# Kernel tuning notes

Hardware: AMD Instinct MI355X
Metric: run time of the kernel (lower is better)

Reference implementation:

```python
import jax, jax.numpy as jnp
import numpy as np

B, H, E, K, O = 16384, 4096, 8, 2, 1
H2 = H // 2


def setup_inputs() -> dict:
    key = jax.random.key(0)
    ks = jax.random.split(key, 9)
    s_h = 1.0 / np.sqrt(H)
    s_h2 = 1.0 / np.sqrt(H2)
    return {
        "x": jax.random.normal(ks[0], (B, H), dtype=jnp.float32),
        # stacked expert weights
        "We1": jax.random.uniform(ks[1], (E, H, H2), jnp.float32, -s_h, s_h),
        "be1": jax.random.uniform(ks[2], (E, H2), jnp.float32, -s_h, s_h),
        "We2": jax.random.uniform(ks[3], (E, H2, O), jnp.float32, -s_h2, s_h2),
        "be2": jax.random.uniform(ks[4], (E, O), jnp.float32, -s_h2, s_h2),
        # gate weights
        "Wg1": jax.random.uniform(ks[5], (H, H2), jnp.float32, -s_h, s_h),
        "bg1": jax.random.uniform(ks[6], (H2,), jnp.float32, -s_h, s_h),
        "Wg2": jax.random.uniform(ks[7], (H2, E), jnp.float32, -s_h2, s_h2),
        "bg2": jax.random.uniform(ks[8], (E,), jnp.float32, -s_h2, s_h2),
    }


def reference(x, We1, be1, We2, be2, Wg1, bg1, Wg2, bg2):
    # gating: Linear -> ReLU -> Linear -> softmax (dropout is identity in eval)
    gh = jax.nn.relu(x @ Wg1 + bg1)                      # [B, H2]
    gate_probs = jax.nn.softmax(gh @ Wg2 + bg2, axis=-1)  # [B, E]
    top_p, top_idx = jax.lax.top_k(gate_probs, K)        # [B, K]
    top_p = top_p / jnp.sum(top_p, axis=-1, keepdims=True)
    # dense all-experts MLP (faithful to original's redundant compute)
    h = jax.nn.relu(jnp.einsum('bh,ehd->bed', x, We1) + be1)  # [B, E, H2]
    expert_out = jnp.einsum('bed,edo->beo', h, We2) + be2     # [B, E, O]
    # gather top-k experts per token and combine
    sel = jnp.take_along_axis(expert_out, top_idx[:, :, None], axis=1)  # [B, K, O]
    return jnp.sum(sel * top_p[:, :, None], axis=1)  # [B, O]
```

## Files before the change

### kernel.cpp

```cpp
#include <hip/hip_runtime.h>
#include <hip/hip_bf16.h>
#include <stdint.h>


#define B_DIM  16384
#define H_DIM  4096
#define H2_DIM 2048
#define E_DIM  8

typedef __attribute__((ext_vector_type(8))) short short8;
typedef __attribute__((ext_vector_type(4))) float f32x4;

static __device__ __forceinline__ unsigned int bf16_rn(float f) {
    unsigned int u = __builtin_bit_cast(unsigned int, f);
    u += 0x7FFFu + ((u >> 16) & 1u);
    return u >> 16;
}
static __device__ __forceinline__ float bf16f(unsigned int h) {
    unsigned int u = h << 16;
    return __builtin_bit_cast(float, u);
}

static __device__ __forceinline__ void gload_lds16(const void* g, void* l) {
    __builtin_amdgcn_global_load_lds(
        (const __attribute__((address_space(1))) unsigned int*)g,
        (__attribute__((address_space(3))) unsigned int*)l,
        16, 0, 0);
}

__global__ __launch_bounds__(256) void build_xA_panels(
    const float* __restrict__ x, unsigned short* __restrict__ panA)
{
    const int t = blockIdx.x, bm = blockIdx.y, tid = threadIdx.x;
    const size_t ubase = (size_t)(bm * 64 + t) * 2 * 8192;
#pragma unroll
    for (int u = 0; u < 8; ++u) {
        const int gid = u * 256 + tid;
        const int h = gid >> 10, rem = gid & 1023;
        const int row = rem >> 2, slot = rem & 3;
        const int kslot = slot ^ ((row >> 1) & 3);
        const float* s = x + (size_t)(bm * 256 + row) * H_DIM
                           + t * 64 + h * 32 + kslot * 8;
        f32x4 a = ((const f32x4*)s)[0], b = ((const f32x4*)s)[1];
        uint4 o;
        o.x = bf16_rn(a[0]) | (bf16_rn(a[1]) << 16);
        o.y = bf16_rn(a[2]) | (bf16_rn(a[3]) << 16);
        o.z = bf16_rn(b[0]) | (bf16_rn(b[1]) << 16);
        o.w = bf16_rn(b[2]) | (bf16_rn(b[3]) << 16);
        *(uint4*)(panA + ubase + (size_t)h * 8192 + row * 32 + slot * 8) = o;
    }
}

__global__ __launch_bounds__(256) void build_xA_panels_hl(
    const float* __restrict__ x, unsigned short* __restrict__ panA,
    unsigned short* __restrict__ panAl)
{
    const int t = blockIdx.x, bm = blockIdx.y, tid = threadIdx.x;
    const size_t ubase = (size_t)(bm * 64 + t) * 2 * 8192;
#pragma unroll
    for (int u = 0; u < 8; ++u) {
        const int gid = u * 256 + tid;
        const int h = gid >> 10, rem = gid & 1023;
        const int row = rem >> 2, slot = rem & 3;
        const int kslot = slot ^ ((row >> 1) & 3);
        const float* s = x + (size_t)(bm * 256 + row) * H_DIM
                           + t * 64 + h * 32 + kslot * 8;
        f32x4 a = ((const f32x4*)s)[0], b = ((const f32x4*)s)[1];
        unsigned int hb[8], lb[8];
        float v[8] = {a[0], a[1], a[2], a[3], b[0], b[1], b[2], b[3]};
#pragma unroll
        for (int q = 0; q < 8; ++q) {
            hb[q] = bf16_rn(v[q]);
            lb[q] = bf16_rn(v[q] - bf16f(hb[q]));
        }
        uint4 oh, ol;
        oh.x = hb[0] | (hb[1] << 16); oh.y = hb[2] | (hb[3] << 16);
        oh.z = hb[4] | (hb[5] << 16); oh.w = hb[6] | (hb[7] << 16);
        ol.x = lb[0] | (lb[1] << 16); ol.y = lb[2] | (lb[3] << 16);
        ol.z = lb[4] | (lb[5] << 16); ol.w = lb[6] | (lb[7] << 16);
        const size_t idx = ubase + (size_t)h * 8192 + row * 32 + slot * 8;
        *(uint4*)(panA + idx)  = oh;
        *(uint4*)(panAl + idx) = ol;
    }
}

__global__ __launch_bounds__(256) void build_w1B_panels(
    const float* __restrict__ We1, unsigned short* __restrict__ panB)
{
    __shared__ unsigned short tile[64][72];
    const int dblk = blockIdx.x, t = blockIdx.y, e = blockIdx.z;
    const int tid = threadIdx.x;
    {
        const int kr = tid >> 2, c0 = (tid & 3) * 16;
        const float* s = We1 + ((size_t)e * H_DIM + t * 64 + kr) * H2_DIM
                             + dblk * 64 + c0;
#pragma unroll
        for (int q = 0; q < 4; ++q) {
            f32x4 v = ((const f32x4*)s)[q];
            tile[kr][c0 + q * 4 + 0] = (unsigned short)bf16_rn(v[0]);
            tile[kr][c0 + q * 4 + 1] = (unsigned short)bf16_rn(v[1]);
            tile[kr][c0 + q * 4 + 2] = (unsigned short)bf16_rn(v[2]);
            tile[kr][c0 + q * 4 + 3] = (unsigned short)bf16_rn(v[3]);
        }
    }
    __syncthreads();
    const int nbG = e * 8 + (dblk >> 2);
    const int col = tid >> 2, slot = tid & 3;
    const int colg = (dblk & 3) * 64 + col;
    const int kslot = slot ^ ((colg >> 1) & 3);
#pragma unroll
    for (int hh = 0; hh < 2; ++hh) {
        const int kl = hh * 32 + kslot * 8;
        uint4 o;
        o.x = (unsigned int)tile[kl + 0][col] | ((unsigned int)tile[kl + 1][col] << 16);
        o.y = (unsigned int)tile[kl + 2][col] | ((unsigned int)tile[kl + 3][col] << 16);
        o.z = (unsigned int)tile[kl + 4][col] | ((unsigned int)tile[kl + 5][col] << 16);
        o.w = (unsigned int)tile[kl + 6][col] | ((unsigned int)tile[kl + 7][col] << 16);
        *(uint4*)(panB + (((size_t)nbG * 64 + t) * 2 + hh) * 8192
                        + colg * 32 + slot * 8) = o;
    }
}

__global__ __launch_bounds__(256) void build_wg1_panels(
    const float* __restrict__ Wg1, unsigned short* __restrict__ panBgh,
    unsigned short* __restrict__ panBgl)
{
    __shared__ unsigned short tileH[64][72];
    __shared__ unsigned short tileL[64][72];
    const int dblk = blockIdx.x, t = blockIdx.y;
    const int tid = threadIdx.x;
    {
        const int kr = tid >> 2, c0 = (tid & 3) * 16;
        const float* s = Wg1 + ((size_t)t * 64 + kr) * H2_DIM + dblk * 64 + c0;
#pragma unroll
        for (int q = 0; q < 4; ++q) {
            f32x4 v = ((const f32x4*)s)[q];
#pragma unroll
            for (int j = 0; j < 4; ++j) {
                const unsigned int hb = bf16_rn(v[j]);
                tileH[kr][c0 + q * 4 + j] = (unsigned short)hb;
                tileL[kr][c0 + q * 4 + j] =
                    (unsigned short)bf16_rn(v[j] - bf16f(hb));
            }
        }
    }
    __syncthreads();
    const int nbG = dblk >> 1;
    const int col = tid >> 2, slot = tid & 3;
    const int colg = (dblk & 1) * 64 + col;
    const int kslot = slot ^ ((colg >> 1) & 3);
#pragma unroll
    for (int hh = 0; hh < 2; ++hh) {
        const int kl = hh * 32 + kslot * 8;
        uint4 oh, ol;
        oh.x = (unsigned int)tileH[kl + 0][col] | ((unsigned int)tileH[kl + 1][col] << 16);
        oh.y = (unsigned int)tileH[kl + 2][col] | ((unsigned int)tileH[kl + 3][col] << 16);
        oh.z = (unsigned int)tileH[kl + 4][col] | ((unsigned int)tileH[kl + 5][col] << 16);
        oh.w = (unsigned int)tileH[kl + 6][col] | ((unsigned int)tileH[kl + 7][col] << 16);
        ol.x = (unsigned int)tileL[kl + 0][col] | ((unsigned int)tileL[kl + 1][col] << 16);
        ol.y = (unsigned int)tileL[kl + 2][col] | ((unsigned int)tileL[kl + 3][col] << 16);
        ol.z = (unsigned int)tileL[kl + 4][col] | ((unsigned int)tileL[kl + 5][col] << 16);
        ol.w = (unsigned int)tileL[kl + 6][col] | ((unsigned int)tileL[kl + 7][col] << 16);
        const size_t idx = (((size_t)nbG * 64 + t) * 2 + hh) * 4096
                         + colg * 32 + slot * 8;
        *(uint4*)(panBgh + idx) = oh;
        *(uint4*)(panBgl + idx) = ol;
    }
}

__global__ __launch_bounds__(256, 3) void moe_gate_panel(
    const unsigned short* __restrict__ panA, const unsigned short* __restrict__ panAl,
    const unsigned short* __restrict__ panBgh, const unsigned short* __restrict__ panBgl,
    const float* __restrict__ bg1, const float* __restrict__ Wg2,
    float* __restrict__ gpart)
{
    __shared__ short lAh[4096], lAl[4096];
    __shared__ short lBh[4096], lBl[4096];
    __shared__ float lW2[128 * 8];
    __shared__ float gred[2][128][8];

    const int tid  = threadIdx.x;
    const int lane = tid & 63;
    const int wv   = tid >> 6;
    const int wm   = wv >> 1;
    const int wn   = wv & 1;
    const int nb = blockIdx.x;
    const int bm = blockIdx.y;
    const int dbase = nb * 128;

    const char* AhB = (const char*)panA  + ((size_t)(bm >> 1) << 21)
                                         + ((size_t)(bm & 1) << 13);
    const char* AlB = (const char*)panAl + ((size_t)(bm >> 1) << 21)
                                         + ((size_t)(bm & 1) << 13);
    const char* BhB = (const char*)panBgh + ((size_t)nb << 20);
    const char* BlB = (const char*)panBgl + ((size_t)nb << 20);

    {
        const f32x4* s = reinterpret_cast<const f32x4*>(Wg2 + (size_t)dbase * 8);
        reinterpret_cast<f32x4*>(lW2)[tid] = s[tid];
    }

    const int rA = wm * 64 + (lane & 15);
    const int offA = rA * 64 + ((((lane >> 4)) ^ ((rA >> 1) & 3)) << 4);
    const int rB = wn * 64 + (lane & 15);
    const int offB = rB * 64 + ((((lane >> 4)) ^ ((rB >> 1) & 3)) << 4);

    f32x4 acc[4][4];
#pragma unroll
    for (int i = 0; i < 4; ++i)
#pragma unroll
        for (int j = 0; j < 4; ++j) acc[i][j] = (f32x4){0.f, 0.f, 0.f, 0.f};

#define GRD8(BASE, OFF) \
    (*reinterpret_cast<const short8*>(reinterpret_cast<const char*>(BASE) + (OFF)))

    for (int t = 0; t < 128; ++t) {
        __syncthreads();
        {
            const char* ua = AhB + ((size_t)t << 14);
            gload_lds16(ua + tid * 16,        (char*)lAh + wv * 1024);
            gload_lds16(ua + 4096 + tid * 16, (char*)lAh + 4096 + wv * 1024);
            const char* ul = AlB + ((size_t)t << 14);
            gload_lds16(ul + tid * 16,        (char*)lAl + wv * 1024);
            gload_lds16(ul + 4096 + tid * 16, (char*)lAl + 4096 + wv * 1024);
            const char* ub = BhB + ((size_t)t << 13);
            gload_lds16(ub + tid * 16,        (char*)lBh + wv * 1024);
            gload_lds16(ub + 4096 + tid * 16, (char*)lBh + 4096 + wv * 1024);
            const char* vb = BlB + ((size_t)t << 13);
            gload_lds16(vb + tid * 16,        (char*)lBl + wv * 1024);
            gload_lds16(vb + 4096 + tid * 16, (char*)lBl + 4096 + wv * 1024);
        }
        __syncthreads();

        short8 ah[4], al[4], bh[4], bl[4];
#pragma unroll
        for (int i = 0; i < 4; ++i) {
            ah[i] = GRD8(lAh, offA + i * 1024);
            al[i] = GRD8(lAl, offA + i * 1024);
        }
#pragma unroll
        for (int n = 0; n < 4; ++n) {
            bh[n] = GRD8(lBh, offB + n * 1024);
            bl[n] = GRD8(lBl, offB + n * 1024);
        }
        __builtin_amdgcn_s_setprio(1);
#pragma unroll
        for (int i = 0; i < 4; ++i)
#pragma unroll
            for (int n = 0; n < 4; ++n) {
                acc[i][n] = __builtin_amdgcn_mfma_f32_16x16x32_bf16(ah[i], bh[n], acc[i][n], 0, 0, 0);
                acc[i][n] = __builtin_amdgcn_mfma_f32_16x16x32_bf16(ah[i], bl[n], acc[i][n], 0, 0, 0);
                acc[i][n] = __builtin_amdgcn_mfma_f32_16x16x32_bf16(al[i], bh[n], acc[i][n], 0, 0, 0);
            }
        __builtin_amdgcn_s_setprio(0);
    }
#undef GRD8

    const int c = lane & 15, g = lane >> 4;
    float bgv[4];
#pragma unroll
    for (int ni = 0; ni < 4; ++ni) bgv[ni] = bg1[dbase + wn * 64 + ni * 16 + c];
#pragma unroll
    for (int mi = 0; mi < 4; ++mi) {
#pragma unroll
        for (int r = 0; r < 4; ++r) {
            float gv[4];
#pragma unroll
            for (int ni = 0; ni < 4; ++ni)
                gv[ni] = fmaxf(acc[mi][ni][r] + bgv[ni], 0.f);
#pragma unroll
            for (int e8 = 0; e8 < 8; ++e8) {
                float tsum = 0.f;
#pragma unroll
                for (int ni = 0; ni < 4; ++ni)
                    tsum = fmaf(gv[ni], lW2[(wn * 64 + ni * 16 + c) * 8 + e8], tsum);
                tsum += __shfl_xor(tsum, 1);
                tsum += __shfl_xor(tsum, 2);
                tsum += __shfl_xor(tsum, 4);
                tsum += __shfl_xor(tsum, 8);
                if (c == e8) gred[wn][wm * 64 + mi * 16 + g * 4 + r][e8] = tsum;
            }
        }
    }
    __syncthreads();
    {
        const int row = tid & 127;
        const int ebase = (tid >> 7) * 4;
        const int b = bm * 128 + row;
#pragma unroll
        for (int i = 0; i < 4; ++i) {
            const int e8 = ebase + i;
            gpart[(size_t)b * 128 + nb * 8 + e8] =
                gred[0][row][e8] + gred[1][row][e8];
        }
    }
}

__global__ void route_zero(int* __restrict__ cnt) {
    if (threadIdx.x < E_DIM) cnt[threadIdx.x] = 0;
}

__global__ __launch_bounds__(256) void moe_logits_topk(
    const float* __restrict__ gpart, const float* __restrict__ bg2,
    int* __restrict__ sel, float* __restrict__ w2f,
    int* __restrict__ cnt, int* __restrict__ tokenlist)
{
    const int b = blockIdx.x * 256 + threadIdx.x;
    float logit[8];
#pragma unroll
    for (int e = 0; e < 8; ++e) logit[e] = bg2[e];
    const float* gp = gpart + (size_t)b * 128;
#pragma unroll
    for (int cN = 0; cN < 16; ++cN)
#pragma unroll
        for (int e = 0; e < 8; ++e) logit[e] += gp[cN * 8 + e];

    int i1 = 0; float m1 = logit[0];
#pragma unroll
    for (int e = 1; e < 8; ++e) if (logit[e] > m1) { m1 = logit[e]; i1 = e; }
    int i2 = -1; float m2 = -3.4e38f;
#pragma unroll
    for (int e = 0; e < 8; ++e) if (e != i1 && logit[e] > m2) { m2 = logit[e]; i2 = e; }

    sel[b] = i1 | (i2 << 8);
    w2f[b] = expf(m2 - m1);
    const int p1 = atomicAdd(&cnt[i1], 1);
    tokenlist[i1 * B_DIM + p1] = (b << 1);
    const int p2 = atomicAdd(&cnt[i2], 1);
    tokenlist[i2 * B_DIM + p2] = (b << 1) | 1;
}

__global__ void moe_tiletab(
    const int* __restrict__ cnt, int* __restrict__ tileE,
    int* __restrict__ tileB, int* __restrict__ nTiles)
{
    if (threadIdx.x == 0) {
        int tot = 0;
        for (int e = 0; e < E_DIM; ++e) {
            const int nt = (cnt[e] + 127) >> 7;
            for (int j = 0; j < nt; ++j) { tileE[tot] = e; tileB[tot] = j; ++tot; }
        }
        *nTiles = tot;
    }
}

__global__ __launch_bounds__(512, 4) void moe_expert_sparse(
    const unsigned short* __restrict__ panA, const unsigned short* __restrict__ panB,
    const float* __restrict__ be1, const float* __restrict__ We2,
    const int* __restrict__ tileE, const int* __restrict__ tileB,
    const int* __restrict__ nTiles, const int* __restrict__ cnt,
    const int* __restrict__ tokenlist, float* __restrict__ esel)
{
    __shared__ short lA[3][4096];
    __shared__ short lB[3][8192];
    __shared__ float red[4][128];
    __shared__ int   tokbuf[128];

    const int tix = blockIdx.y;
    if (tix >= *nTiles) return;
    const int chunk = blockIdx.x;

    const int tid  = threadIdx.x;
    const int lane = tid & 63;
    const int wv   = tid >> 6;
    const int wm   = wv >> 2;
    const int wn   = wv & 3;

    const int e  = tileE[tix];
    const int tb = tileB[tix];
    const int ce = cnt[e];
    const int nb = e * 8 + chunk;
    const int dbase = chunk * 256;

    if (tid < 128) {
        const int gi = tb * 128 + tid;
        tokbuf[tid] = (gi < ce) ? tokenlist[e * B_DIM + gi] : -1;
    }
    __syncthreads();

    const int rawT = tokbuf[tid >> 2];
    const int tokv = ((rawT < 0) ? tokbuf[0] : rawT) >> 1;
    const int trow = tokv & 255;
    const int lr = tid >> 2, ls = tid & 3;
    const int sslot = ls ^ ((lr >> 1) & 3) ^ ((trow >> 1) & 3);
    const char* Asrc = (const char*)panA + ((size_t)(tokv >> 8) << 21)
                     + trow * 64 + sslot * 16;
    const char* Bbase = (const char*)panB + ((size_t)nb << 21);

#define STAGE(TT, CC) do {                                                     \
    gload_lds16(Asrc + ((size_t)(TT) << 14), (char*)&lA[CC][0] + wv * 1024);   \
    const char* ub_ = Bbase + ((size_t)(TT) << 14);                            \
    gload_lds16(ub_ + tid * 16, (char*)&lB[CC][0] + wv * 1024);                \
    gload_lds16(ub_ + 8192 + tid * 16, (char*)&lB[CC][0] + 8192 + wv * 1024);  \
} while (0)

#define RD8(BASE, OFF) \
    (*reinterpret_cast<const short8*>(reinterpret_cast<const char*>(BASE) + (OFF)))

    const int rA = wm * 64 + (lane & 15);
    const int offA = rA * 64 + ((((lane >> 4)) ^ ((rA >> 1) & 3)) << 4);
    const int rB = wn * 64 + (lane & 15);
    const int offB = rB * 64 + ((((lane >> 4)) ^ ((rB >> 1) & 3)) << 4);

    f32x4 acc[4][4];
#pragma unroll
    for (int i = 0; i < 4; ++i)
#pragma unroll
        for (int j = 0; j < 4; ++j) acc[i][j] = (f32x4){0.f, 0.f, 0.f, 0.f};

    STAGE(0, 0);
    STAGE(1, 1);
    asm volatile("s_waitcnt vmcnt(3)");
    __builtin_amdgcn_s_barrier();

#define ITER(CUR, NXT, TN) do {                                                \
    STAGE(TN, NXT);                                                            \
    short8 af_[4], bf_[4];                                                     \
    _Pragma("unroll")                                                          \
    for (int i = 0; i < 4; ++i) af_[i] = RD8(&lA[CUR][0], offA + i * 1024);    \
    _Pragma("unroll")                                                          \
    for (int n = 0; n < 4; ++n) bf_[n] = RD8(&lB[CUR][0], offB + n * 1024);    \
    __builtin_amdgcn_s_setprio(1);                                             \
    _Pragma("unroll")                                                          \
    for (int i = 0; i < 4; ++i)                                                \
        _Pragma("unroll")                                                      \
        for (int n = 0; n < 4; ++n)                                            \
            acc[i][n] = __builtin_amdgcn_mfma_f32_16x16x32_bf16(af_[i], bf_[n], acc[i][n], 0, 0, 0); \
    __builtin_amdgcn_s_setprio(0);                                             \
    asm volatile("s_waitcnt vmcnt(3)");                                        \
    __builtin_amdgcn_s_barrier();                                              \
} while (0)

    for (int t = 0; t < 126; t += 3) {
        ITER(0, 2, t + 2);
        ITER(1, 0, t + 3);
        ITER(2, 1, t + 4);
    }
    ITER(0, 2, 127);
    ITER(1, 0, 127);
    asm volatile("s_waitcnt vmcnt(0)");
#undef ITER
#undef STAGE

    const int cc = lane & 15, g = lane >> 4;
    float w2v[4], b1v[4];
#pragma unroll
    for (int ni = 0; ni < 4; ++ni) {
        const int d = dbase + wn * 64 + ni * 16 + cc;
        b1v[ni] = be1[e * H2_DIM + d];
        w2v[ni] = We2[e * H2_DIM + d];
    }
#pragma unroll
    for (int mi = 0; mi < 4; ++mi) {
#pragma unroll
        for (int r = 0; r < 4; ++r) {
            float s = 0.f;
#pragma unroll
            for (int ni = 0; ni < 4; ++ni) {
                float v = acc[mi][ni][r] + b1v[ni];
                v = fmaxf(v, 0.f);
                s = fmaf(v, w2v[ni], s);
            }
            s += __shfl_xor(s, 1);
            s += __shfl_xor(s, 2);
            s += __shfl_xor(s, 4);
            s += __shfl_xor(s, 8);
            if (cc == 0) red[wn][wm * 64 + mi * 16 + g * 4 + r] = s;
        }
    }
    __syncthreads();
    if (tid < 128) {
        const int r2 = tokbuf[tid];
        if (r2 >= 0) {
            const int tk = r2 >> 1, sl = r2 & 1;
            esel[(size_t)tk * 16 + sl * 8 + chunk] =
                red[0][tid] + red[1][tid] + red[2][tid] + red[3][tid];
        }
    }
}

__global__ __launch_bounds__(256) void moe_finalize_sparse(
    const float* __restrict__ esel, const int* __restrict__ sel,
    const float* __restrict__ w2f, const float* __restrict__ be2,
    float* __restrict__ out)
{
    const int b = blockIdx.x * 256 + threadIdx.x;
    const int s = sel[b];
    const int i1 = s & 255, i2 = (s >> 8) & 255;
    const float w2 = w2f[b];
    const float* ep = esel + (size_t)b * 16;
    float eo1 = be2[i1], eo2 = be2[i2];
#pragma unroll
    for (int c = 0; c < 8; ++c) eo1 += ep[c];
#pragma unroll
    for (int c = 0; c < 8; ++c) eo2 += ep[8 + c];
    out[b] = (eo1 + w2 * eo2) / (1.f + w2);
}

__global__ __launch_bounds__(512, 4) void moe_expert_gemm_128(
    const unsigned short* __restrict__ panA, const unsigned short* __restrict__ panB,
    const float* __restrict__ be1, const float* __restrict__ We2,
    float* __restrict__ epart)
{
    __shared__ short lA[3][4096];
    __shared__ short lB[3][8192];
    __shared__ float red[4][128];

    const int tid  = threadIdx.x;
    const int lane = tid & 63;
    const int wv   = tid >> 6;
    const int wm   = wv >> 2;
    const int wn   = wv & 3;

    const int lin = blockIdx.x;
    const int sb  = lin >> 8, i5 = lin & 255;
    const int sbm = sb & 7, snb = sb >> 3;
    const int xcd = i5 & 7, j5 = i5 >> 3;
    const int bm  = sbm * 16 + (xcd & 1) * 8 + (j5 & 7);
    const int nb  = snb * 16 + (xcd >> 1) * 4 + (j5 >> 3);
    const int e = nb >> 3, chunk = nb & 7;
    const int dbase = chunk * 256;

    const char* Abase = (const char*)panA + ((size_t)(bm >> 1) << 21)
                                          + ((size_t)(bm & 1) << 13);
    const char* Bbase = (const char*)panB + ((size_t)nb << 21);

#define STAGE(TT, CC) do {                                                     \
    const char* ua_ = Abase + ((size_t)(TT) << 14);                            \
    gload_lds16(ua_ + tid * 16, (char*)&lA[CC][0] + wv * 1024);                \
    const char* ub_ = Bbase + ((size_t)(TT) << 14);                            \
    gload_lds16(ub_ + tid * 16, (char*)&lB[CC][0] + wv * 1024);                \
    gload_lds16(ub_ + 8192 + tid * 16, (char*)&lB[CC][0] + 8192 + wv * 1024);  \
} while (0)

#define RD8(BASE, OFF) \
    (*reinterpret_cast<const short8*>(reinterpret_cast<const char*>(BASE) + (OFF)))

    const int rA = wm * 64 + (lane & 15);
    const int offA = rA * 64 + ((((lane >> 4)) ^ ((rA >> 1) & 3)) << 4);
    const int rB = wn * 64 + (lane & 15);
    const int offB = rB * 64 + ((((lane >> 4)) ^ ((rB >> 1) & 3)) << 4);

    f32x4 acc[4][4];
#pragma unroll
    for (int i = 0; i < 4; ++i)
#pragma unroll
        for (int j = 0; j < 4; ++j) acc[i][j] = (f32x4){0.f, 0.f, 0.f, 0.f};

    STAGE(0, 0);
    STAGE(1, 1);
    asm volatile("s_waitcnt vmcnt(3)");
    __builtin_amdgcn_s_barrier();

#define ITER(CUR, NXT, TN) do {                                                \
    STAGE(TN, NXT);                                                            \
    short8 af_[4], bf_[4];                                                     \
    _Pragma("unroll")                                                          \
    for (int i = 0; i < 4; ++i) af_[i] = RD8(&lA[CUR][0], offA + i * 1024);    \
    _Pragma("unroll")                                                          \
    for (int n = 0; n < 4; ++n) bf_[n] = RD8(&lB[CUR][0], offB + n * 1024);    \
    __builtin_amdgcn_s_setprio(1);                                             \
    _Pragma("unroll")                                                          \
    for (int i = 0; i < 4; ++i)                                                \
        _Pragma("unroll")                                                      \
        for (int n = 0; n < 4; ++n)                                            \
            acc[i][n] = __builtin_amdgcn_mfma_f32_16x16x32_bf16(af_[i], bf_[n], acc[i][n], 0, 0, 0); \
    __builtin_amdgcn_s_setprio(0);                                             \
    asm volatile("s_waitcnt vmcnt(3)");                                        \
    __builtin_amdgcn_s_barrier();                                              \
} while (0)

    for (int t = 0; t < 126; t += 3) {
        ITER(0, 2, t + 2);
        ITER(1, 0, t + 3);
        ITER(2, 1, t + 4);
    }
    ITER(0, 2, 127);
    ITER(1, 0, 127);
    asm volatile("s_waitcnt vmcnt(0)");
#undef ITER
#undef STAGE

    const int cc = lane & 15, g = lane >> 4;
    float w2v[4], b1v[4];
#pragma unroll
    for (int ni = 0; ni < 4; ++ni) {
        const int d = dbase + wn * 64 + ni * 16 + cc;
        b1v[ni] = be1[e * H2_DIM + d];
        w2v[ni] = We2[e * H2_DIM + d];
    }
#pragma unroll
    for (int mi = 0; mi < 4; ++mi) {
#pragma unroll
        for (int r = 0; r < 4; ++r) {
            float s = 0.f;
#pragma unroll
            for (int ni = 0; ni < 4; ++ni) {
                float v = acc[mi][ni][r] + b1v[ni];
                v = fmaxf(v, 0.f);
                s = fmaf(v, w2v[ni], s);
            }
            s += __shfl_xor(s, 1);
            s += __shfl_xor(s, 2);
            s += __shfl_xor(s, 4);
            s += __shfl_xor(s, 8);
            if (cc == 0) red[wn][wm * 64 + mi * 16 + g * 4 + r] = s;
        }
    }
    __syncthreads();
    if (tid < 128) {
        const int b = bm * 128 + tid;
        epart[((size_t)b * E_DIM + e) * 8 + chunk] =
            red[0][tid] + red[1][tid] + red[2][tid] + red[3][tid];
    }
}

__global__ __launch_bounds__(256, 2) void moe_gate_gemm(
    const float* __restrict__ x, const float* __restrict__ Wg1,
    const float* __restrict__ bg1, const float* __restrict__ Wg2,
    float* __restrict__ gpart)
{
    __shared__ short lAh[128 * 64], lAl[128 * 64];
    __shared__ short lBh[128 * 64], lBl[128 * 64];
    __shared__ float lW2[128 * 8];
    __shared__ float gred[2][128][8];

    const int tid  = threadIdx.x;
    const int lane = tid & 63;
    const int wm = (tid >> 6) >> 1, wn = (tid >> 6) & 1;
    const int nb = blockIdx.x, bm = blockIdx.y;
    const int dbase = nb * 128;

    const float* Asrc = x + (size_t)bm * 128 * H_DIM;
    const float* Bsrc = Wg1 + dbase;

    {
        const f32x4* s = reinterpret_cast<const f32x4*>(Wg2 + (size_t)dbase * 8);
        reinterpret_cast<f32x4*>(lW2)[tid] = s[tid];
    }

    f32x4 acc[4][4];
#pragma unroll
    for (int i = 0; i < 4; ++i)
#pragma unroll
        for (int j = 0; j < 4; ++j) acc[i][j] = (f32x4){0.f, 0.f, 0.f, 0.f};

    const int arow0 = tid >> 4, af4 = tid & 15;
    const int bn = tid & 127, bkc0 = tid >> 7;

    for (int k0 = 0; k0 < H_DIM; k0 += 64) {
        __syncthreads();
#pragma unroll
        for (int j = 0; j < 8; ++j) {
            const int row = arow0 + j * 16;
            const float* p = Asrc + (size_t)row * H_DIM + k0 + af4 * 4;
            float a[4] = {p[0], p[1], p[2], p[3]};
            unsigned int hb[4], lb[4];
#pragma unroll
            for (int q = 0; q < 4; ++q) {
                hb[q] = bf16_rn(a[q]);
                lb[q] = bf16_rn(a[q] - bf16f(hb[q]));
            }
            const int byte = row * 128 + ((af4 * 8) ^ ((row & 7) << 4));
            *reinterpret_cast<uint2*>(reinterpret_cast<char*>(lAh) + byte) =
                make_uint2(hb[0] | (hb[1] << 16), hb[2] | (hb[3] << 16));
            *reinterpret_cast<uint2*>(reinterpret_cast<char*>(lAl) + byte) =
                make_uint2(lb[0] | (lb[1] << 16), lb[2] | (lb[3] << 16));
        }
#pragma unroll
        for (int j = 0; j < 4; ++j) {
            const int kc = bkc0 + 2 * j;
            const float* p = Bsrc + (size_t)(k0 + kc * 8) * H2_DIM + bn;
            unsigned int hb[8], lb[8];
#pragma unroll
            for (int q = 0; q < 8; ++q) {
                float v = p[(size_t)q * H2_DIM];
                hb[q] = bf16_rn(v);
                lb[q] = bf16_rn(v - bf16f(hb[q]));
            }
            const int byte = bn * 128 + ((kc * 16) ^ ((bn & 7) << 4));
            *reinterpret_cast<uint4*>(reinterpret_cast<char*>(lBh) + byte) =
                make_uint4(hb[0] | (hb[1] << 16), hb[2] | (hb[3] << 16),
                           hb[4] | (hb[5] << 16), hb[6] | (hb[7] << 16));
            *reinterpret_cast<uint4*>(reinterpret_cast<char*>(lBl) + byte) =
                make_uint4(lb[0] | (lb[1] << 16), lb[2] | (lb[3] << 16),
                           lb[4] | (lb[5] << 16), lb[6] | (lb[7] << 16));
        }
        __syncthreads();
#pragma unroll
        for (int kk = 0; kk < 2; ++kk) {
            const int kbyte = kk * 64 + ((lane >> 4) << 4);
            short8 ah[4], al[4], bh[4], bl[4];
#pragma unroll
            for (int mi = 0; mi < 4; ++mi) {
                const int r = wm * 64 + mi * 16 + (lane & 15);
                const int off = r * 128 + (kbyte ^ ((r & 7) << 4));
                ah[mi] = *reinterpret_cast<const short8*>(reinterpret_cast<const char*>(lAh) + off);
                al[mi] = *reinterpret_cast<const short8*>(reinterpret_cast<const char*>(lAl) + off);
            }
#pragma unroll
            for (int ni = 0; ni < 4; ++ni) {
                const int r = wn * 64 + ni * 16 + (lane & 15);
                const int off = r * 128 + (kbyte ^ ((r & 7) << 4));
                bh[ni] = *reinterpret_cast<const short8*>(reinterpret_cast<const char*>(lBh) + off);
                bl[ni] = *reinterpret_cast<const short8*>(reinterpret_cast<const char*>(lBl) + off);
            }
#pragma unroll
            for (int mi = 0; mi < 4; ++mi)
#pragma unroll
                for (int ni = 0; ni < 4; ++ni) {
                    acc[mi][ni] = __builtin_amdgcn_mfma_f32_16x16x32_bf16(ah[mi], bh[ni], acc[mi][ni], 0, 0, 0);
                    acc[mi][ni] = __builtin_amdgcn_mfma_f32_16x16x32_bf16(ah[mi], bl[ni], acc[mi][ni], 0, 0, 0);
                    acc[mi][ni] = __builtin_amdgcn_mfma_f32_16x16x32_bf16(al[mi], bh[ni], acc[mi][ni], 0, 0, 0);
                }
        }
    }

    const int c = lane & 15, g = lane >> 4;
    float bgv[4];
#pragma unroll
    for (int ni = 0; ni < 4; ++ni) bgv[ni] = bg1[dbase + wn * 64 + ni * 16 + c];
#pragma unroll
    for (int mi = 0; mi < 4; ++mi) {
#pragma unroll
        for (int r = 0; r < 4; ++r) {
            float gv[4];
#pragma unroll
            for (int ni = 0; ni < 4; ++ni)
                gv[ni] = fmaxf(acc[mi][ni][r] + bgv[ni], 0.f);
#pragma unroll
            for (int e8 = 0; e8 < 8; ++e8) {
                float t = 0.f;
#pragma unroll
                for (int ni = 0; ni < 4; ++ni)
                    t = fmaf(gv[ni], lW2[(wn * 64 + ni * 16 + c) * 8 + e8], t);
                t += __shfl_xor(t, 1);
                t += __shfl_xor(t, 2);
                t += __shfl_xor(t, 4);
                t += __shfl_xor(t, 8);
                if (c == e8) gred[wn][wm * 64 + mi * 16 + g * 4 + r][e8] = t;
            }
        }
    }
    __syncthreads();
    {
        const int row = tid & 127;
        const int ebase = (tid >> 7) * 4;
        const int b = bm * 128 + row;
#pragma unroll
        for (int i = 0; i < 4; ++i) {
            const int e8 = ebase + i;
            gpart[(size_t)b * 128 + nb * 8 + e8] = gred[0][row][e8] + gred[1][row][e8];
        }
    }
}

__global__ __launch_bounds__(256, 2) void moe_expert_gemm(
    const float* __restrict__ x, const float* __restrict__ We1,
    const float* __restrict__ be1, const float* __restrict__ We2,
    float* __restrict__ epart)
{
    __shared__ short lA[128 * 64];
    __shared__ short lB[128 * 64];
    __shared__ float red[2][128];

    const int tid  = threadIdx.x;
    const int lane = tid & 63;
    const int wm   = (tid >> 6) >> 1;
    const int wn   = (tid >> 6) & 1;
    const int nb = blockIdx.x, bm = blockIdx.y;
    const int e = nb >> 4, chunk = nb & 15;
    const int dbase = chunk * 128;

    const float* Asrc = x + (size_t)bm * 128 * H_DIM;
    const float* Bsrc = We1 + (size_t)e * H_DIM * H2_DIM + dbase;

    f32x4 acc[4][4];
#pragma unroll
    for (int i = 0; i < 4; ++i)
#pragma unroll
        for (int j = 0; j < 4; ++j) acc[i][j] = (f32x4){0.f, 0.f, 0.f, 0.f};

    const int arow0 = tid >> 4, af4 = tid & 15;
    const int bn = tid & 127, bkc0 = tid >> 7;

    for (int k0 = 0; k0 < H_DIM; k0 += 64) {
        __syncthreads();
#pragma unroll
        for (int j = 0; j < 8; ++j) {
            const int row = arow0 + j * 16;
            const float* p = Asrc + (size_t)row * H_DIM + k0 + af4 * 4;
            float a0 = p[0], a1 = p[1], a2 = p[2], a3 = p[3];
            uint2 wv2;
            wv2.x = bf16_rn(a0) | (bf16_rn(a1) << 16);
            wv2.y = bf16_rn(a2) | (bf16_rn(a3) << 16);
            const int byte = row * 128 + ((af4 * 8) ^ ((row & 7) << 4));
            *reinterpret_cast<uint2*>(reinterpret_cast<char*>(lA) + byte) = wv2;
        }
#pragma unroll
        for (int j = 0; j < 4; ++j) {
            const int kc = bkc0 + 2 * j;
            const float* p = Bsrc + (size_t)(k0 + kc * 8) * H2_DIM + bn;
            uint4 wv4;
            wv4.x = bf16_rn(p[0])          | (bf16_rn(p[H2_DIM])     << 16);
            wv4.y = bf16_rn(p[2 * H2_DIM]) | (bf16_rn(p[3 * H2_DIM]) << 16);
            wv4.z = bf16_rn(p[4 * H2_DIM]) | (bf16_rn(p[5 * H2_DIM]) << 16);
            wv4.w = bf16_rn(p[6 * H2_DIM]) | (bf16_rn(p[7 * H2_DIM]) << 16);
            const int byte = bn * 128 + ((kc * 16) ^ ((bn & 7) << 4));
            *reinterpret_cast<uint4*>(reinterpret_cast<char*>(lB) + byte) = wv4;
        }
        __syncthreads();
#pragma unroll
        for (int kk = 0; kk < 2; ++kk) {
            const int kbyte = kk * 64 + ((lane >> 4) << 4);
            short8 af[4], bfr[4];
#pragma unroll
            for (int mi = 0; mi < 4; ++mi) {
                const int r = wm * 64 + mi * 16 + (lane & 15);
                af[mi] = *reinterpret_cast<const short8*>(
                    reinterpret_cast<const char*>(lA) + r * 128 + (kbyte ^ ((r & 7) << 4)));
            }
#pragma unroll
            for (int ni = 0; ni < 4; ++ni) {
                const int r = wn * 64 + ni * 16 + (lane & 15);
                bfr[ni] = *reinterpret_cast<const short8*>(
                    reinterpret_cast<const char*>(lB) + r * 128 + (kbyte ^ ((r & 7) << 4)));
            }
#pragma unroll
            for (int mi = 0; mi < 4; ++mi)
#pragma unroll
                for (int ni = 0; ni < 4; ++ni)
                    acc[mi][ni] = __builtin_amdgcn_mfma_f32_16x16x32_bf16(
                        af[mi], bfr[ni], acc[mi][ni], 0, 0, 0);
        }
    }

    const int c = lane & 15, g = lane >> 4;
    float w2v[4], b1v[4];
#pragma unroll
    for (int ni = 0; ni < 4; ++ni) {
        const int d = dbase + wn * 64 + ni * 16 + c;
        b1v[ni] = be1[e * H2_DIM + d];
        w2v[ni] = We2[e * H2_DIM + d];
    }
#pragma unroll
    for (int mi = 0; mi < 4; ++mi) {
#pragma unroll
        for (int r = 0; r < 4; ++r) {
            float s = 0.f;
#pragma unroll
            for (int ni = 0; ni < 4; ++ni) {
                float v = acc[mi][ni][r] + b1v[ni];
                v = fmaxf(v, 0.f);
                s = fmaf(v, w2v[ni], s);
            }
            s += __shfl_xor(s, 1);
            s += __shfl_xor(s, 2);
            s += __shfl_xor(s, 4);
            s += __shfl_xor(s, 8);
            if (c == 0) red[wn][wm * 64 + mi * 16 + g * 4 + r] = s;
        }
    }
    __syncthreads();
    if (tid < 128) {
        const int b = bm * 128 + tid;
        epart[((size_t)b * E_DIM + e) * 16 + chunk] = red[0][tid] + red[1][tid];
    }
}

template <int NC>
__global__ __launch_bounds__(256) void moe_finalize(
    const float* __restrict__ gpart, const float* __restrict__ epart,
    const float* __restrict__ bg2, const float* __restrict__ be2,
    float* __restrict__ out)
{
    const int b = blockIdx.x * 256 + threadIdx.x;
    float logit[8];
#pragma unroll
    for (int e = 0; e < 8; ++e) logit[e] = bg2[e];
    const float* gp = gpart + (size_t)b * 128;
#pragma unroll
    for (int cN = 0; cN < 16; ++cN)
#pragma unroll
        for (int e = 0; e < 8; ++e) logit[e] += gp[cN * 8 + e];

    float eo[8];
    const float* ep = epart + (size_t)b * E_DIM * NC;
#pragma unroll
    for (int e = 0; e < 8; ++e) {
        float s = be2[e];
#pragma unroll
        for (int cN = 0; cN < NC; ++cN) s += ep[e * NC + cN];
        eo[e] = s;
    }

    int i1 = 0; float m1 = logit[0];
#pragma unroll
    for (int e = 1; e < 8; ++e) if (logit[e] > m1) { m1 = logit[e]; i1 = e; }
    int i2 = -1; float m2 = -3.4e38f;
#pragma unroll
    for (int e = 0; e < 8; ++e) if (e != i1 && logit[e] > m2) { m2 = logit[e]; i2 = e; }

    const float w2 = expf(m2 - m1);
    out[b] = (eo[i1] + w2 * eo[i2]) / (1.f + w2);
}

extern "C" void kernel_launch(void* const* d_in, const int* in_sizes, int n_in,
                              void* d_out, int out_size, void* d_ws, size_t ws_size,
                              hipStream_t stream) {
    (void)in_sizes; (void)n_in; (void)out_size;
    const float* x   = (const float*)d_in[0];
    const float* We1 = (const float*)d_in[1];
    const float* be1 = (const float*)d_in[2];
    const float* We2 = (const float*)d_in[3];
    const float* be2 = (const float*)d_in[4];
    const float* Wg1 = (const float*)d_in[5];
    const float* bg1 = (const float*)d_in[6];
    const float* Wg2 = (const float*)d_in[7];
    const float* bg2 = (const float*)d_in[8];
    float* out = (float*)d_out;

    char* ws = (char*)d_ws;
    size_t off = 0;
    float* gpart = (float*)(ws + off);                  off += (size_t)B_DIM * 128 * 4;
    float* epart = (float*)(ws + off);                  off += (size_t)B_DIM * 128 * 4;
    unsigned short* panA = (unsigned short*)(ws + off); off += (size_t)B_DIM * H_DIM * 2;
    unsigned short* panB = (unsigned short*)(ws + off); off += (size_t)E_DIM * H2_DIM * H_DIM * 2;
    const size_t NEED2 = off;
    unsigned short* panAl  = (unsigned short*)(ws + off); off += (size_t)B_DIM * H_DIM * 2;
    unsigned short* panBgh = (unsigned short*)(ws + off); off += (size_t)H2_DIM * H_DIM * 2;
    unsigned short* panBgl = (unsigned short*)(ws + off); off += (size_t)H2_DIM * H_DIM * 2;
    int*   cnt       = (int*)(ws + off);   off += 256;
    int*   nTiles    = (int*)(ws + off);   off += 256;
    int*   tileE     = (int*)(ws + off);   off += 272 * 4;
    int*   tileB     = (int*)(ws + off);   off += 272 * 4;
    int*   sel       = (int*)(ws + off);   off += (size_t)B_DIM * 4;
    float* w2f       = (float*)(ws + off); off += (size_t)B_DIM * 4;
    int*   tokenlist = (int*)(ws + off);   off += (size_t)E_DIM * B_DIM * 4;
    const size_t NEED1 = off;
    float* esel = epart;

    if (ws_size >= NEED1) {
        build_xA_panels_hl<<<dim3(64, 64), 256, 0, stream>>>(x, panA, panAl);
        build_wg1_panels<<<dim3(32, 64), 256, 0, stream>>>(Wg1, panBgh, panBgl);
        build_w1B_panels<<<dim3(32, 64, 8), 256, 0, stream>>>(We1, panB);
        route_zero<<<1, 64, 0, stream>>>(cnt);
        moe_gate_panel<<<dim3(16, 128), 256, 0, stream>>>(panA, panAl, panBgh, panBgl,
                                                          bg1, Wg2, gpart);
        moe_logits_topk<<<64, 256, 0, stream>>>(gpart, bg2, sel, w2f, cnt, tokenlist);
        moe_tiletab<<<1, 64, 0, stream>>>(cnt, tileE, tileB, nTiles);
        moe_expert_sparse<<<dim3(8, 264), 512, 0, stream>>>(
            panA, panB, be1, We2, tileE, tileB, nTiles, cnt, tokenlist, esel);
        moe_finalize_sparse<<<64, 256, 0, stream>>>(esel, sel, w2f, be2, out);
    } else if (ws_size >= NEED2) {
        build_xA_panels<<<dim3(64, 64), 256, 0, stream>>>(x, panA);
        build_w1B_panels<<<dim3(32, 64, 8), 256, 0, stream>>>(We1, panB);
        moe_expert_gemm_128<<<8192, 512, 0, stream>>>(panA, panB, be1, We2, epart);
        moe_gate_gemm<<<dim3(16, 128), 256, 0, stream>>>(x, Wg1, bg1, Wg2, gpart);
        moe_finalize<8><<<64, 256, 0, stream>>>(gpart, epart, bg2, be2, out);
    } else {
        moe_expert_gemm<<<dim3(128, 128), 256, 0, stream>>>(x, We1, be1, We2, epart);
        moe_gate_gemm<<<dim3(16, 128), 256, 0, stream>>>(x, Wg1, bg1, Wg2, gpart);
        moe_finalize<16><<<64, 256, 0, stream>>>(gpart, epart, bg2, be2, out);
    }
}
```

Measured before the change: 1.651 ms.

## Double-buffer LDS tiles in gate GEMM to overlap global loads with MFMA

Converts the gate panel GEMM main loop to a double-buffered LDS scheme. The next k-tile is issued via global_load_lds into the alternate buffer before computing on the current one, with a single vmcnt wait and barrier per iteration instead of two syncthreads. LDS usage doubles, so launch bounds drop from 3 to 2 blocks per CU, which lowers occupancy. The last iteration redundantly reloads tile 127.

```diff
diff --git a/kernel.cpp b/kernel.cpp
--- a/kernel.cpp
+++ b/kernel.cpp
@@ -168,14 +168,14 @@
     }
 }
 
-__global__ __launch_bounds__(256, 3) void moe_gate_panel(
+__global__ __launch_bounds__(256, 2) void moe_gate_panel(
     const unsigned short* __restrict__ panA, const unsigned short* __restrict__ panAl,
     const unsigned short* __restrict__ panBgh, const unsigned short* __restrict__ panBgl,
     const float* __restrict__ bg1, const float* __restrict__ Wg2,
     float* __restrict__ gpart)
 {
-    __shared__ short lAh[4096], lAl[4096];
-    __shared__ short lBh[4096], lBl[4096];
+    __shared__ short lAh[2][4096], lAl[2][4096];
+    __shared__ short lBh[2][4096], lBl[2][4096];
     __shared__ float lW2[128 * 8];
     __shared__ float gred[2][128][8];
 
@@ -214,47 +214,59 @@
 #define GRD8(BASE, OFF) \
     (*reinterpret_cast<const short8*>(reinterpret_cast<const char*>(BASE) + (OFF)))
 
-    for (int t = 0; t < 128; ++t) {
-        __syncthreads();
-        {
-            const char* ua = AhB + ((size_t)t << 14);
-            gload_lds16(ua + tid * 16,        (char*)lAh + wv * 1024);
-            gload_lds16(ua + 4096 + tid * 16, (char*)lAh + 4096 + wv * 1024);
-            const char* ul = AlB + ((size_t)t << 14);
-            gload_lds16(ul + tid * 16,        (char*)lAl + wv * 1024);
-            gload_lds16(ul + 4096 + tid * 16, (char*)lAl + 4096 + wv * 1024);
-            const char* ub = BhB + ((size_t)t << 13);
-            gload_lds16(ub + tid * 16,        (char*)lBh + wv * 1024);
-            gload_lds16(ub + 4096 + tid * 16, (char*)lBh + 4096 + wv * 1024);
-            const char* vb = BlB + ((size_t)t << 13);
-            gload_lds16(vb + tid * 16,        (char*)lBl + wv * 1024);
-            gload_lds16(vb + 4096 + tid * 16, (char*)lBl + 4096 + wv * 1024);
-        }
-        __syncthreads();
-
-        short8 ah[4], al[4], bh[4], bl[4];
-#pragma unroll
-        for (int i = 0; i < 4; ++i) {
-            ah[i] = GRD8(lAh, offA + i * 1024);
-            al[i] = GRD8(lAl, offA + i * 1024);
-        }
-#pragma unroll
-        for (int n = 0; n < 4; ++n) {
-            bh[n] = GRD8(lBh, offB + n * 1024);
-            bl[n] = GRD8(lBl, offB + n * 1024);
-        }
-        __builtin_amdgcn_s_setprio(1);
-#pragma unroll
-        for (int i = 0; i < 4; ++i)
-#pragma unroll
-            for (int n = 0; n < 4; ++n) {
-                acc[i][n] = __builtin_amdgcn_mfma_f32_16x16x32_bf16(ah[i], bh[n], acc[i][n], 0, 0, 0);
-                acc[i][n] = __builtin_amdgcn_mfma_f32_16x16x32_bf16(ah[i], bl[n], acc[i][n], 0, 0, 0);
-                acc[i][n] = __builtin_amdgcn_mfma_f32_16x16x32_bf16(al[i], bh[n], acc[i][n], 0, 0, 0);
-            }
-        __builtin_amdgcn_s_setprio(0);
-    }
-#undef GRD8
+#define GSTAGE(TT, CC) do {                                                    \
+    const char* ua = AhB + ((size_t)(TT) << 14);                               \
+    gload_lds16(ua + tid * 16,        (char*)&lAh[CC][0] + wv * 1024);         \
+    gload_lds16(ua + 4096 + tid * 16, (char*)&lAh[CC][0] + 4096 + wv * 1024);  \
+    const char* ul = AlB + ((size_t)(TT) << 14);                               \
+    gload_lds16(ul + tid * 16,        (char*)&lAl[CC][0] + wv * 1024);         \
+    gload_lds16(ul + 4096 + tid * 16, (char*)&lAl[CC][0] + 4096 + wv * 1024);  \
+    const char* ub = BhB + ((size_t)(TT) << 13);                               \
+    gload_lds16(ub + tid * 16,        (char*)&lBh[CC][0] + wv * 1024);         \
+    gload_lds16(ub + 4096 + tid * 16, (char*)&lBh[CC][0] + 4096 + wv * 1024);  \
+    const char* vb = BlB + ((size_t)(TT) << 13);                               \
+    gload_lds16(vb + tid * 16,        (char*)&lBl[CC][0] + wv * 1024);         \
+    gload_lds16(vb + 4096 + tid * 16, (char*)&lBl[CC][0] + 4096 + wv * 1024);  \
+} while (0)
+
+#define GITER(CC, TN) do {                                                     \
+    GSTAGE(TN, (CC) ^ 1);                                                      \
+    short8 ah[4], al[4], bh[4], bl[4];                                         \
+    _Pragma("unroll")                                                          \
+    for (int i = 0; i < 4; ++i) {                                              \
+        ah[i] = GRD8(&lAh[CC][0], offA + i * 1024);                            \
+        al[i] = GRD8(&lAl[CC][0], offA + i * 1024);                            \
+    }                                                                          \
+    _Pragma("unroll")                                                          \
+    for (int n = 0; n < 4; ++n) {                                              \
+        bh[n] = GRD8(&lBh[CC][0], offB + n * 1024);                            \
+        bl[n] = GRD8(&lBl[CC][0], offB + n * 1024);                            \
+    }                                                                          \
+    __builtin_amdgcn_s_setprio(1);                                             \
+    _Pragma("unroll")                                                          \
+    for (int i = 0; i < 4; ++i)                                                \
+        _Pragma("unroll")                                                      \
+        for (int n = 0; n < 4; ++n) {                                          \
+            acc[i][n] = __builtin_amdgcn_mfma_f32_16x16x32_bf16(ah[i], bh[n], acc[i][n], 0, 0, 0); \
+            acc[i][n] = __builtin_amdgcn_mfma_f32_16x16x32_bf16(ah[i], bl[n], acc[i][n], 0, 0, 0); \
+            acc[i][n] = __builtin_amdgcn_mfma_f32_16x16x32_bf16(al[i], bh[n], acc[i][n], 0, 0, 0); \
+        }                                                                      \
+    __builtin_amdgcn_s_setprio(0);                                             \
+    asm volatile("s_waitcnt vmcnt(0)");                                        \
+    __builtin_amdgcn_s_barrier();                                              \
+} while (0)
+
+    GSTAGE(0, 0);
+    asm volatile("s_waitcnt vmcnt(0)");
+    __builtin_amdgcn_s_barrier();
+
+    for (int t = 0; t < 128; t += 2) {
+        GITER(0, t + 1);
+        GITER(1, (t + 2 < 128) ? t + 2 : 127);
+    }
+    asm volatile("s_waitcnt vmcnt(0)");
+#undef GITER
+#undef GSTAGE
 
     const int c = lane & 15, g = lane >> 4;
     float bgv[4];
```

Result: slower. 1.732 ms (+4.9%).
